# Performance work log

Measured on AMD Instinct MI355X. Metric: run time of the kernel, lower is better.

The kernel has to match this reference:

```python
import jax, jax.numpy as jnp
import numpy as np

EPS = 1e-06


def setup_inputs() -> dict:
    key = jax.random.key(0)
    k1, k2, k3 = jax.random.split(key, 3)
    B, H, S, D = 4, 16, 4096, 64
    query = jax.random.normal(k1, (B, H, S, D), dtype=jnp.float32)
    key_t = jax.random.normal(k2, (B, H, S, D), dtype=jnp.float32)
    value = jax.random.normal(k3, (B, H, S, D), dtype=jnp.float32)
    return {"query": query, "key": key_t, "value": value}


def _cosformer_features(x, cos_idx, sin_idx):
    # x: [B,H,S,D]; cos_idx/sin_idx: [S,1] -> features [B,H,S,2D]
    x_relu = jax.nn.relu(x)
    return jnp.concatenate([x_relu * cos_idx, x_relu * sin_idx], axis=-1)


def reference(query, key, value):
    B, H, S, D = query.shape
    query = query / jnp.sqrt(jnp.asarray(D, dtype=query.dtype))
    # idx = (pi/2) * [1..S]; angles divided by seq_len
    ang = (jnp.pi / 2) * jnp.arange(1, S + 1, dtype=query.dtype) / S  # [S]
    cos_idx = jnp.cos(ang)[:, None]  # [S,1]
    sin_idx = jnp.sin(ang)[:, None]  # [S,1]
    q_cs = _cosformer_features(query, cos_idx, sin_idx)  # [B,H,S,2D]
    k_cs = _cosformer_features(key, cos_idx, sin_idx)    # [B,H,S,2D]
    # norm: 1 / clamp(q_cs . sum_l(k_cs), eps)
    k_sum = jnp.sum(k_cs, axis=-2)  # [B,H,2D]
    norm = 1.0 / jnp.maximum(jnp.einsum('bhld,bhd->bhl', q_cs, k_sum), EPS)  # [B,H,S]
    # linear attention: KV aggregation then query projection
    kv = jnp.einsum('bhld,bhlm->bhdm', k_cs, value)  # [B,H,2D,D]
    out = jnp.einsum('bhld,bhdm->bhlm', q_cs, kv) * norm[..., None]  # [B,H,S,D]
    return out
```

## Files before the change

kernel.cpp:

```cpp
#include <hip/hip_runtime.h>
#include <hip/hip_bf16.h>
#include <math.h>

#define BHN    64
#define SEQ    4096
#define DIM    64
#define NCHUNK 16
#define CHUNK  (SEQ / NCHUNK)
#define KSTEP  64
#define NIT    (CHUNK / KSTEP)
#define KVF    (128 * DIM)
#define STRIDE_C ((size_t)BHN * KVF + (size_t)BHN * 128)
#define KSBASE ((size_t)BHN * KVF)
#define FRAGH  10240
#define LPAD   72

typedef __bf16 bf16x8v __attribute__((ext_vector_type(8)));
typedef float  f32x4v  __attribute__((ext_vector_type(4)));

__device__ inline f32x4v mfma16(bf16x8v a, bf16x8v b, f32x4v c) {
    return __builtin_amdgcn_mfma_f32_16x16x32_bf16(a, b, c, 0, 0, 0);
}

__device__ inline unsigned pk2(float a, float b) {
    __hip_bfloat162 t(__float2bfloat16(a), __float2bfloat16(b));
    return *(unsigned*)&t;
}

__device__ inline int swz(int d, int col) { return col ^ (4 * ((d >> 2) & 7)); }

template<int USE_ATOMIC>
__global__ __launch_bounds__(512) void cosformer_kv_mfma(
    const float* __restrict__ K, const float* __restrict__ V,
    float* __restrict__ part)
{
    __shared__ ushort ktc[64][LPAD];
    __shared__ ushort kts[64][LPAD];
    __shared__ ushort vt [64][LPAD];

    const int bh    = blockIdx.x / NCHUNK;
    const int chunk = blockIdx.x % NCHUNK;
    const int row0  = chunk * CHUNK;
    const float* Kb = K + (size_t)bh * SEQ * DIM;
    const float* Vb = V + (size_t)bh * SEQ * DIM;

    const int tid = threadIdx.x;
    const int dq = (tid & 15) * 4;
    const int g  = tid >> 4;
    const int lane = tid & 63;
    const int w    = tid >> 6;
    const int frow = lane & 15;
    const int kgrp = lane >> 4;

    f32x4v acc[5];
    #pragma unroll
    for (int t = 0; t < 5; ++t) acc[t] = (f32x4v){0.f, 0.f, 0.f, 0.f};

    bf16x8v onef;
    #pragma unroll
    for (int j = 0; j < 8; ++j) onef[j] = (frow == 0) ? (__bf16)1.0f : (__bf16)0.0f;

    float4 s0[4], s1[4];

    auto LOADS = [&](int it, float4* r) {
        const float* kp = Kb + (size_t)(row0 + it * KSTEP + 2 * g) * DIM + dq;
        const float* vp = Vb + (size_t)(row0 + it * KSTEP + 2 * g) * DIM + dq;
        r[0] = *(const float4*)kp;
        r[1] = *(const float4*)(kp + DIM);
        r[2] = *(const float4*)vp;
        r[3] = *(const float4*)(vp + DIM);
    };

    auto WRITES = [&](int it, const float4* r) {
        const int l0 = row0 + it * KSTEP + 2 * g;
        const float CC = 1.5707963267948966f / (float)SEQ;
        float s0v, c0, s1v, c1;
        __sincosf(CC * (float)(l0 + 1), &s0v, &c0);
        __sincosf(CC * (float)(l0 + 2), &s1v, &c1);
        float k0[4] = {r[0].x, r[0].y, r[0].z, r[0].w};
        float k1[4] = {r[1].x, r[1].y, r[1].z, r[1].w};
        float v0[4] = {r[2].x, r[2].y, r[2].z, r[2].w};
        float v1[4] = {r[3].x, r[3].y, r[3].z, r[3].w};
        #pragma unroll
        for (int i = 0; i < 4; ++i) {
            const int d = dq + i;
            const int c = swz(d, g);
            float r0 = fmaxf(k0[i], 0.f), r1 = fmaxf(k1[i], 0.f);
            ((unsigned*)&ktc[d][0])[c] = pk2(r0 * c0,  r1 * c1);
            ((unsigned*)&kts[d][0])[c] = pk2(r0 * s0v, r1 * s1v);
            ((unsigned*)&vt [d][0])[c] = pk2(v0[i],    v1[i]);
        }
    };

    LOADS(0, s0);
    LOADS(1, s1);
    WRITES(0, s0);
    LOADS(2, s0);
    __syncthreads();

    const ushort (*ap)[LPAD] = (w < 4) ? ktc : kts;
    const int d0 = (w & 3) * 16 + frow;

    #pragma unroll
    for (int it = 0; it < NIT; ++it) {
        #pragma unroll
        for (int ks = 0; ks < 2; ++ks) {
            const int cb = ks * 16 + kgrp * 4;
            bf16x8v a = *(const bf16x8v*)&ap[d0][2 * swz(d0, cb)];
            #pragma unroll
            for (int nt = 0; nt < 4; ++nt) {
                const int dn = nt * 16 + frow;
                bf16x8v b = *(const bf16x8v*)&vt[dn][2 * swz(dn, cb)];
                acc[nt] = mfma16(a, b, acc[nt]);
            }
            acc[4] = mfma16(a, onef, acc[4]);
        }
        __syncthreads();
        if (it + 1 < NIT) {
            WRITES(it + 1, ((it + 1) & 1) ? s1 : s0);
            if (it + 3 < NIT) LOADS(it + 3, ((it + 3) & 1) ? s1 : s0);
            __syncthreads();
        }
    }

    const int fb = w * 16 + kgrp * 4;
    if (USE_ATOMIC) {
        float* pb = part + (size_t)bh * KVF;
        float* ps = part + KSBASE + bh * 128;
        #pragma unroll
        for (int nt = 0; nt < 4; ++nt)
            #pragma unroll
            for (int r = 0; r < 4; ++r)
                atomicAdd(&pb[(size_t)(fb + r) * DIM + nt * 16 + frow], acc[nt][r]);
        if (frow == 0)
            #pragma unroll
            for (int r = 0; r < 4; ++r) atomicAdd(&ps[fb + r], acc[4][r]);
    } else {
        float* pb = part + STRIDE_C * chunk + (size_t)bh * KVF;
        float* ps = part + STRIDE_C * chunk + KSBASE + bh * 128;
        #pragma unroll
        for (int nt = 0; nt < 4; ++nt)
            #pragma unroll
            for (int r = 0; r < 4; ++r)
                pb[(size_t)(fb + r) * DIM + nt * 16 + frow] = acc[nt][r];
        if (frow == 0)
            #pragma unroll
            for (int r = 0; r < 4; ++r) ps[fb + r] = acc[4][r];
    }
}

template<int NC>
__global__ __launch_bounds__(256) void reduce_pack(
    const float* __restrict__ part, __hip_bfloat16* __restrict__ bfrag)
{
    size_t o = (size_t)blockIdx.x * 256 + threadIdx.x;
    float s = 0.f;
    #pragma unroll
    for (int c = 0; c < NC; ++c) s += part[(size_t)c * STRIDE_C + o];
    if (o < KSBASE) {
        int head = (int)(o >> 13);
        int r = (int)(o & 8191);
        int k = r >> 6, n = r & 63;
        int t = n >> 4, ks = k >> 5, lg = (k >> 3) & 3, j = k & 7;
        int lane = lg * 16 + (n & 15);
        bfrag[(size_t)head * FRAGH + (size_t)(((t * 4 + ks) * 64 + lane) * 8 + j)] =
            __float2bfloat16(s);
    } else {
        int r = (int)(o - KSBASE);
        int head = r >> 7, k = r & 127;
        int ks = k >> 5, lg = (k >> 3) & 3, j = k & 7;
        bfrag[(size_t)head * FRAGH + (size_t)(((16 + ks) * 64 + lg * 16) * 8 + j)] =
            __float2bfloat16(s);
    }
}

__global__ __launch_bounds__(256) void cosformer_out_mfma(
    const float* __restrict__ Q, const __hip_bfloat16* __restrict__ bfrag,
    float* __restrict__ out)
{
    __shared__ __hip_bfloat16 sb[FRAGH];
    const int head = blockIdx.x >> 3;
    const int tile = blockIdx.x & 7;
    const int tid  = threadIdx.x;

    {
        const float4* src = (const float4*)(bfrag + (size_t)head * FRAGH);
        float4* dst = (float4*)sb;
        #pragma unroll
        for (int i = 0; i < 5; ++i) dst[tid + 256 * i] = src[tid + 256 * i];
    }

    const int lane = tid & 63;
    const int w    = tid >> 6;
    const int mrow = lane & 15;
    const int kgrp = lane >> 4;

    const float* Qb = Q + (size_t)head * SEQ * DIM;
    float*       Ob = out + (size_t)head * SEQ * DIM;
    const int rowblk = tile * 512;

    float4 qb[2][4];
    #pragma unroll
    for (int m = 0; m < 2; ++m) {
        const float4* qr = (const float4*)(Qb + (size_t)(rowblk + w * 32 + m * 16 + mrow) * DIM);
        qb[m][0] = qr[kgrp * 2];
        qb[m][1] = qr[kgrp * 2 + 1];
        qb[m][2] = qr[8 + kgrp * 2];
        qb[m][3] = qr[8 + kgrp * 2 + 1];
    }

    __syncthreads();

    #pragma unroll
    for (int g = 0; g < 4; ++g) {
        const int base = rowblk + (g * 4 + w) * 32;

        bf16x8v af[2][4];
        #pragma unroll
        for (int m = 0; m < 2; ++m) {
            int arow = base + m * 16 + mrow;
            float ang = 1.5707963267948966f * (float)(arow + 1) / (float)SEQ;
            float sn, cn;
            __sincosf(ang, &sn, &cn);
            float crs = cn * 0.125f, srs = sn * 0.125f;
            float lo[8] = {qb[m][0].x, qb[m][0].y, qb[m][0].z, qb[m][0].w,
                           qb[m][1].x, qb[m][1].y, qb[m][1].z, qb[m][1].w};
            float hi[8] = {qb[m][2].x, qb[m][2].y, qb[m][2].z, qb[m][2].w,
                           qb[m][3].x, qb[m][3].y, qb[m][3].z, qb[m][3].w};
            #pragma unroll
            for (int j = 0; j < 8; ++j) {
                float rl = fmaxf(lo[j], 0.f);
                float rh = fmaxf(hi[j], 0.f);
                af[m][0][j] = (__bf16)(rl * crs);
                af[m][1][j] = (__bf16)(rh * crs);
                af[m][2][j] = (__bf16)(rl * srs);
                af[m][3][j] = (__bf16)(rh * srs);
            }
        }

        if (g < 3) {
            #pragma unroll
            for (int m = 0; m < 2; ++m) {
                const float4* qr = (const float4*)(Qb + (size_t)(rowblk + ((g + 1) * 4 + w) * 32 + m * 16 + mrow) * DIM);
                qb[m][0] = qr[kgrp * 2];
                qb[m][1] = qr[kgrp * 2 + 1];
                qb[m][2] = qr[8 + kgrp * 2];
                qb[m][3] = qr[8 + kgrp * 2 + 1];
            }
        }

        f32x4v acc[2][5];
        #pragma unroll
        for (int m = 0; m < 2; ++m)
            #pragma unroll
            for (int t = 0; t < 5; ++t)
                acc[m][t] = (f32x4v){0.f, 0.f, 0.f, 0.f};

        #pragma unroll
        for (int t = 0; t < 5; ++t)
            #pragma unroll
            for (int ks = 0; ks < 4; ++ks) {
                bf16x8v bf = *(const bf16x8v*)&sb[(size_t)(((t * 4 + ks) * 64 + lane) * 8)];
                acc[0][t] = mfma16(af[0][ks], bf, acc[0][t]);
                acc[1][t] = mfma16(af[1][ks], bf, acc[1][t]);
            }

        #pragma unroll
        for (int m = 0; m < 2; ++m) {
            #pragma unroll
            for (int r = 0; r < 4; ++r) {
                float den = __shfl(acc[m][4][r], lane & 48, 64);
                float invd = 1.0f / fmaxf(den, 1e-6f);
                int row = base + m * 16 + kgrp * 4 + r;
                float* op = Ob + (size_t)row * DIM + mrow;
                op[0]  = acc[m][0][r] * invd;
                op[16] = acc[m][1][r] * invd;
                op[32] = acc[m][2][r] * invd;
                op[48] = acc[m][3][r] * invd;
            }
        }
    }
}

extern "C" void kernel_launch(void* const* d_in, const int* in_sizes, int n_in,
                              void* d_out, int out_size, void* d_ws, size_t ws_size,
                              hipStream_t stream) {
    const float* Q = (const float*)d_in[0];
    const float* K = (const float*)d_in[1];
    const float* V = (const float*)d_in[2];
    float* out = (float*)d_out;
    float* ws  = (float*)d_ws;

    const size_t frag_bytes = (size_t)FRAGH * BHN * sizeof(__hip_bfloat16);
    const size_t need_full  = (size_t)NCHUNK * STRIDE_C * sizeof(float) + frag_bytes;

    if (ws_size >= need_full) {
        float* part = ws;
        __hip_bfloat16* bfrag = (__hip_bfloat16*)(ws + (size_t)NCHUNK * STRIDE_C);
        hipMemsetAsync(bfrag, 0, frag_bytes, stream);
        hipLaunchKernelGGL((cosformer_kv_mfma<0>), dim3(BHN * NCHUNK), dim3(512), 0, stream,
                           K, V, part);
        hipLaunchKernelGGL((reduce_pack<NCHUNK>), dim3((int)(STRIDE_C / 256)), dim3(256), 0, stream,
                           part, bfrag);
        hipLaunchKernelGGL(cosformer_out_mfma, dim3(BHN * 8), dim3(256), 0, stream,
                           Q, bfrag, out);
    } else {
        float* part = ws;
        __hip_bfloat16* bfrag = (__hip_bfloat16*)(ws + STRIDE_C);
        hipMemsetAsync(part, 0, STRIDE_C * sizeof(float), stream);
        hipMemsetAsync(bfrag, 0, frag_bytes, stream);
        hipLaunchKernelGGL((cosformer_kv_mfma<1>), dim3(BHN * NCHUNK), dim3(512), 0, stream,
                           K, V, part);
        hipLaunchKernelGGL((reduce_pack<1>), dim3((int)(STRIDE_C / 256)), dim3(256), 0, stream,
                           part, bfrag);
        hipLaunchKernelGGL(cosformer_out_mfma, dim3(BHN * 8), dim3(256), 0, stream,
                           Q, bfrag, out);
    }
}
```

Measured before the change: 79.22 us.

## Double-buffer LDS tiles, deepen register prefetch, and halve sequence chunks

Turns the shared-memory K/V tiles into double buffers so the next tile is written while the current one is consumed, which drops one of the two barriers per iteration. Global loads are prefetched three tiles ahead instead of two, using a third register set. The sequence split per head goes from 16 chunks to 8, so each block runs more iterations and there are fewer partial results to reduce. The cost is double the LDS use, more register pressure, and half as many blocks, which may lower occupancy.

```diff
diff --git a/kernel.cpp b/kernel.cpp
--- a/kernel.cpp
+++ b/kernel.cpp
@@ -5,7 +5,7 @@
 #define BHN    64
 #define SEQ    4096
 #define DIM    64
-#define NCHUNK 16
+#define NCHUNK 8
 #define CHUNK  (SEQ / NCHUNK)
 #define KSTEP  64
 #define NIT    (CHUNK / KSTEP)
@@ -34,9 +34,9 @@
     const float* __restrict__ K, const float* __restrict__ V,
     float* __restrict__ part)
 {
-    __shared__ ushort ktc[64][LPAD];
-    __shared__ ushort kts[64][LPAD];
-    __shared__ ushort vt [64][LPAD];
+    __shared__ ushort ktc[2][64][LPAD];
+    __shared__ ushort kts[2][64][LPAD];
+    __shared__ ushort vtt[2][64][LPAD];
 
     const int bh    = blockIdx.x / NCHUNK;
     const int chunk = blockIdx.x % NCHUNK;
@@ -60,7 +60,7 @@
     #pragma unroll
     for (int j = 0; j < 8; ++j) onef[j] = (frow == 0) ? (__bf16)1.0f : (__bf16)0.0f;
 
-    float4 s0[4], s1[4];
+    float4 sA[4], sB[4], sC[4];
 
     auto LOADS = [&](int it, float4* r) {
         const float* kp = Kb + (size_t)(row0 + it * KSTEP + 2 * g) * DIM + dq;
@@ -71,7 +71,7 @@
         r[3] = *(const float4*)(vp + DIM);
     };
 
-    auto WRITES = [&](int it, const float4* r) {
+    auto WRITES = [&](int it, const float4* r, int buf) {
         const int l0 = row0 + it * KSTEP + 2 * g;
         const float CC = 1.5707963267948966f / (float)SEQ;
         float s0v, c0, s1v, c1;
@@ -86,23 +86,39 @@
             const int d = dq + i;
             const int c = swz(d, g);
             float r0 = fmaxf(k0[i], 0.f), r1 = fmaxf(k1[i], 0.f);
-            ((unsigned*)&ktc[d][0])[c] = pk2(r0 * c0,  r1 * c1);
-            ((unsigned*)&kts[d][0])[c] = pk2(r0 * s0v, r1 * s1v);
-            ((unsigned*)&vt [d][0])[c] = pk2(v0[i],    v1[i]);
+            ((unsigned*)&ktc[buf][d][0])[c] = pk2(r0 * c0,  r1 * c1);
+            ((unsigned*)&kts[buf][d][0])[c] = pk2(r0 * s0v, r1 * s1v);
+            ((unsigned*)&vtt[buf][d][0])[c] = pk2(v0[i],    v1[i]);
         }
     };
 
-    LOADS(0, s0);
-    LOADS(1, s1);
-    WRITES(0, s0);
-    LOADS(2, s0);
+    auto LOADS_SEL = [&](int it) {
+        int sel = it % 3;
+        if (sel == 0) LOADS(it, sA);
+        else if (sel == 1) LOADS(it, sB);
+        else LOADS(it, sC);
+    };
+    auto WRITES_SEL = [&](int it, int buf) {
+        int sel = it % 3;
+        if (sel == 0) WRITES(it, sA, buf);
+        else if (sel == 1) WRITES(it, sB, buf);
+        else WRITES(it, sC, buf);
+    };
+
+    LOADS_SEL(0);
+    LOADS_SEL(1);
+    LOADS_SEL(2);
+    WRITES_SEL(0, 0);
+    LOADS_SEL(3);
     __syncthreads();
 
-    const ushort (*ap)[LPAD] = (w < 4) ? ktc : kts;
     const int d0 = (w & 3) * 16 + frow;
 
     #pragma unroll
     for (int it = 0; it < NIT; ++it) {
+        const int buf = it & 1;
+        const ushort (*ap)[LPAD] = (w < 4) ? ktc[buf] : kts[buf];
+        const ushort (*bp)[LPAD] = vtt[buf];
         #pragma unroll
         for (int ks = 0; ks < 2; ++ks) {
             const int cb = ks * 16 + kgrp * 4;
@@ -110,17 +126,16 @@
             #pragma unroll
             for (int nt = 0; nt < 4; ++nt) {
                 const int dn = nt * 16 + frow;
-                bf16x8v b = *(const bf16x8v*)&vt[dn][2 * swz(dn, cb)];
+                bf16x8v b = *(const bf16x8v*)&bp[dn][2 * swz(dn, cb)];
                 acc[nt] = mfma16(a, b, acc[nt]);
             }
             acc[4] = mfma16(a, onef, acc[4]);
         }
+        if (it + 1 < NIT) {
+            WRITES_SEL(it + 1, buf ^ 1);
+            if (it + 4 < NIT) LOADS_SEL(it + 4);
+        }
         __syncthreads();
-        if (it + 1 < NIT) {
-            WRITES(it + 1, ((it + 1) & 1) ? s1 : s0);
-            if (it + 3 < NIT) LOADS(it + 3, ((it + 3) & 1) ? s1 : s0);
-            __syncthreads();
-        }
     }
 
     const int fb = w * 16 + kgrp * 4;
```

Result: faster. 70.04 us (-11.6%).

## Halve KV chunk count and issue all chunk loads up front with lighter barriers

Applied to the files above, without the earlier changes.

Cuts the KV kernel's sequence split from 16 to 8 chunks, so each block covers 8 KSTEP iterations. All eight iterations' K/V global loads are now issued into registers at the start, and the rolling double-buffer prefetch is gone. __syncthreads is replaced by a raw s_barrier that waits only on LDS counters, avoiding waits on outstanding global loads, and launch bounds request 2 blocks per CU. The aim is more memory-level parallelism and fewer partial sums to reduce, at the cost of much higher register pressure and half as many blocks.

```diff
diff --git a/kernel.cpp b/kernel.cpp
--- a/kernel.cpp
+++ b/kernel.cpp
@@ -5,7 +5,7 @@
 #define BHN    64
 #define SEQ    4096
 #define DIM    64
-#define NCHUNK 16
+#define NCHUNK 8
 #define CHUNK  (SEQ / NCHUNK)
 #define KSTEP  64
 #define NIT    (CHUNK / KSTEP)
@@ -27,16 +27,22 @@
     return *(unsigned*)&t;
 }
 
+__device__ __forceinline__ void barrier_noflush() {
+    asm volatile("s_waitcnt lgkmcnt(0)" ::: "memory");
+    __builtin_amdgcn_s_barrier();
+    asm volatile("" ::: "memory");
+}
+
 __device__ inline int swz(int d, int col) { return col ^ (4 * ((d >> 2) & 7)); }
 
 template<int USE_ATOMIC>
-__global__ __launch_bounds__(512) void cosformer_kv_mfma(
+__global__ __launch_bounds__(512, 2) void cosformer_kv_mfma(
     const float* __restrict__ K, const float* __restrict__ V,
     float* __restrict__ part)
 {
     __shared__ ushort ktc[64][LPAD];
     __shared__ ushort kts[64][LPAD];
-    __shared__ ushort vt [64][LPAD];
+    __shared__ ushort vtt[64][LPAD];
 
     const int bh    = blockIdx.x / NCHUNK;
     const int chunk = blockIdx.x % NCHUNK;
@@ -60,7 +66,7 @@
     #pragma unroll
     for (int j = 0; j < 8; ++j) onef[j] = (frow == 0) ? (__bf16)1.0f : (__bf16)0.0f;
 
-    float4 s0[4], s1[4];
+    float4 sA[4], sB[4], sC[4], sD[4], sE[4], sF[4], sG[4], sH[4];
 
     auto LOADS = [&](int it, float4* r) {
         const float* kp = Kb + (size_t)(row0 + it * KSTEP + 2 * g) * DIM + dq;
@@ -88,21 +94,28 @@
             float r0 = fmaxf(k0[i], 0.f), r1 = fmaxf(k1[i], 0.f);
             ((unsigned*)&ktc[d][0])[c] = pk2(r0 * c0,  r1 * c1);
             ((unsigned*)&kts[d][0])[c] = pk2(r0 * s0v, r1 * s1v);
-            ((unsigned*)&vt [d][0])[c] = pk2(v0[i],    v1[i]);
+            ((unsigned*)&vtt[d][0])[c] = pk2(v0[i],    v1[i]);
         }
     };
 
-    LOADS(0, s0);
-    LOADS(1, s1);
-    WRITES(0, s0);
-    LOADS(2, s0);
-    __syncthreads();
-
-    const ushort (*ap)[LPAD] = (w < 4) ? ktc : kts;
+    LOADS(0, sA); LOADS(1, sB); LOADS(2, sC); LOADS(3, sD);
+    LOADS(4, sE); LOADS(5, sF); LOADS(6, sG); LOADS(7, sH);
+
     const int d0 = (w & 3) * 16 + frow;
 
     #pragma unroll
     for (int it = 0; it < NIT; ++it) {
+        if      (it == 0) WRITES(0, sA);
+        else if (it == 1) WRITES(1, sB);
+        else if (it == 2) WRITES(2, sC);
+        else if (it == 3) WRITES(3, sD);
+        else if (it == 4) WRITES(4, sE);
+        else if (it == 5) WRITES(5, sF);
+        else if (it == 6) WRITES(6, sG);
+        else              WRITES(7, sH);
+        barrier_noflush();
+
+        const ushort (*ap)[LPAD] = (w < 4) ? ktc : kts;
         #pragma unroll
         for (int ks = 0; ks < 2; ++ks) {
             const int cb = ks * 16 + kgrp * 4;
@@ -110,17 +123,12 @@
             #pragma unroll
             for (int nt = 0; nt < 4; ++nt) {
                 const int dn = nt * 16 + frow;
-                bf16x8v b = *(const bf16x8v*)&vt[dn][2 * swz(dn, cb)];
+                bf16x8v b = *(const bf16x8v*)&vtt[dn][2 * swz(dn, cb)];
                 acc[nt] = mfma16(a, b, acc[nt]);
             }
             acc[4] = mfma16(a, onef, acc[4]);
         }
-        __syncthreads();
-        if (it + 1 < NIT) {
-            WRITES(it + 1, ((it + 1) & 1) ? s1 : s0);
-            if (it + 3 < NIT) LOADS(it + 3, ((it + 3) & 1) ? s1 : s0);
-            __syncthreads();
-        }
+        barrier_noflush();
     }
 
     const int fb = w * 16 + kgrp * 4;
@@ -209,7 +217,7 @@
         qb[m][3] = qr[8 + kgrp * 2 + 1];
     }
 
-    __syncthreads();
+    barrier_noflush();
 
     #pragma unroll
     for (int g = 0; g < 4; ++g) {
```

Result: faster. 76.82 us (-3.0%).
